# Performance work log

Measured on AMD Instinct MI355X. Metric: run time of the kernel, lower is better.

Reference implementation:

```python
import jax, jax.numpy as jnp
import numpy as np

T, M, K, B, H, L, V = 64, 256, 6, 256, 256, 128, 780
E = T * M
PAD = E  # padding slot in hidden buffer = Lorentz origin

def _to_lorentz_np(s):
    t = np.sqrt(1.0 + (s * s).sum(-1, keepdims=True))
    return np.concatenate([t, s], -1).astype(np.float32)

def setup_inputs() -> dict:
    rng = np.random.default_rng(0)
    def make_nei():
        idx = np.full((T, M, K), PAD, np.int64)
        w = np.zeros((T, M, K), np.float32)
        for t in range(T):
            deg = rng.integers(0, K + 1, size=M)
            if t == 0:
                deg[:] = 0  # no messages exist yet
            mask = np.arange(K)[None, :] < deg[:, None]
            cand = rng.integers(0, max(1, t * M), size=(M, K))  # only already-computed slots
            idx[t] = np.where(mask, cand, PAD)
            w[t] = mask.astype(np.float32)
            w[t, deg == 0, 0] = 1.0  # zero-neighbor case -> use origin padding (as in torch code)
        return idx.astype(np.int32), w
    nei_h_idx, nei_h_w = make_nei()
    nei_o_idx, nei_o_w = make_nei()
    return dict(
        wid=jnp.asarray(rng.integers(0, V, size=(T, M)), jnp.int32),
        nei_h_idx=jnp.asarray(nei_h_idx), nei_h_w=jnp.asarray(nei_h_w),
        nei_o_idx=jnp.asarray(nei_o_idx), nei_o_w=jnp.asarray(nei_o_w),
        batch_idx=jnp.asarray(rng.integers(0, B, size=(T, M)), jnp.int32),
        direction=jnp.asarray(rng.integers(0, 2, size=(T, M)), jnp.int32),
        pred_target=jnp.asarray(rng.integers(0, V, size=(T, M)), jnp.int32),
        root_wid=jnp.asarray(rng.integers(0, V, size=(B,)), jnp.int32),
        root_o_idx=jnp.asarray(rng.integers(0, E, size=(B, K)), jnp.int32),
        root_o_w=jnp.ones((B, K), jnp.float32),
        x_tree_vecs=jnp.asarray(_to_lorentz_np(rng.standard_normal((B, L - 1)) * 0.5)),
        embedding=jnp.asarray(_to_lorentz_np(rng.standard_normal((V, H - 1)) * 0.5)),
        W0=jnp.asarray(rng.standard_normal((H, H)) * 0.02, dtype=jnp.float32),
        b0=jnp.zeros((H,), jnp.float32),
        s0=jnp.asarray(np.log(10.0), jnp.float32),
        W1=jnp.asarray(rng.standard_normal((H, 2 * H - 1)) * 0.02, dtype=jnp.float32),
        b1=jnp.zeros((H,), jnp.float32),
        s1=jnp.asarray(np.log(10.0), jnp.float32),
        wcls=jnp.asarray(_to_lorentz_np(rng.standard_normal((V, H + L - 2)) * 0.5)),
        wbias=jnp.zeros((V,), jnp.float32),
        ucls=jnp.asarray(_to_lorentz_np(rng.standard_normal((2, 2 * H + L - 3)) * 0.5)),
        ubias=jnp.zeros((2,), jnp.float32),
    )

def _llinear(x, W, b, scale):
    # LorentzLinear: affine map, then rescale space part so output stays on the hyperboloid
    x = x @ W.T + b
    xs = x[..., 1:]
    time = jax.nn.sigmoid(x[..., :1]) * jnp.exp(scale) + 1.1
    sq = (time * time - 1.0) / jnp.clip((xs * xs).sum(-1, keepdims=True), 1e-8)
    return jnp.concatenate([time, xs * jnp.sqrt(sq)], -1)

def _mid_point(x, w):
    # Lorentz centroid: weighted mean renormalized to the manifold. x: [...,K,d], w: [...,K]
    ave = jnp.einsum('...k,...kd->...d', w, x) / jnp.clip(w.sum(-1, keepdims=True), 1e-8)
    inner = (ave[..., 1:] ** 2).sum(-1, keepdims=True) - ave[..., :1] ** 2  # <ave,ave>_L
    return ave / jnp.sqrt(jnp.clip(-inner, 1e-8))

def _concat(x, y):
    # hyperbolic concat: keep space parts, recompute time (dim = d1+d2-1)
    time = jnp.sqrt(jnp.clip(x[..., :1] ** 2 + y[..., :1] ** 2 - 1.0, 1e-8))
    return jnp.concatenate([time, x[..., 1:], y[..., 1:]], -1)

def _centroid(x, cls_pts, bias):
    # LorentzCentroidDistance logits: 2 + 2*<x, c>_L + bias
    inner = x[..., 1:] @ cls_pts[:, 1:].T - x[..., :1] * cls_pts[None, :, 0]
    return 2.0 + 2.0 * inner + bias

def _ce(scores, tgt):
    lp = jax.nn.log_softmax(scores, -1)
    return -jnp.take_along_axis(lp, tgt[:, None], axis=-1)[:, 0]

def _forward_core(wid, nei_h_idx, nei_h_w, nei_o_idx, nei_o_w, batch_idx, direction,
                  pred_target, root_wid, root_o_idx, root_o_w, x_tree_vecs, embedding,
                  W0, b0, s0, W1, b1, s1, wcls, wbias, ucls, ubias):
    hbuf0 = jnp.zeros((E + 1, H), jnp.float32).at[:, 0].set(1.0)  # all origin; slot E is padding

    def step(carry, xs_t):
        hbuf, t = carry
        wid_t, idx_t, w_t = xs_t
        cur_x = embedding[wid_t]                      # [M,H]
        h_nei = hbuf[idx_t]                           # [M,K,H] gather of prior messages
        h1 = _llinear(h_nei, W0, b0, s0)              # A0
        h1m = _mid_point(h1, w_t)                     # [M,H]
        new_h = _llinear(_concat(cur_x, h1m), W1, b1, s1)  # A1
        hbuf = jax.lax.dynamic_update_slice(hbuf, new_h, (t * M, 0))
        return (hbuf, t + jnp.int32(1)), new_h

    (hbuf, _), new_h = jax.lax.scan(step, (hbuf0, jnp.int32(0)), (wid, nei_h_idx, nei_h_w))
    new_h = new_h.reshape(E, H)
    cur_x = embedding[wid.reshape(E)]
    cur_o = _mid_point(hbuf[nei_o_idx.reshape(E, K)], nei_o_w.reshape(E, K))
    ctx = x_tree_vecs[batch_idx.reshape(E)]

    # word prediction: roots (origin hidden) + forward-direction messages
    origin = jnp.zeros((B, H), jnp.float32).at[:, 0].set(1.0)
    root_scores = _centroid(_concat(origin, x_tree_vecs), wcls, wbias)   # [B,V]
    msg_scores = _centroid(_concat(new_h, ctx), wcls, wbias)             # [E,V]
    pmask = direction.reshape(E).astype(jnp.float32)
    pt = pred_target.reshape(E)
    pred_loss = (_ce(root_scores, root_wid).sum() + (pmask * _ce(msg_scores, pt)).sum()) / B
    pred_hit = ((jnp.argmax(root_scores, -1) == root_wid).astype(jnp.float32).sum()
                + (pmask * (jnp.argmax(msg_scores, -1) == pt).astype(jnp.float32)).sum())
    pred_acc = pred_hit / (B + pmask.sum())

    # stop prediction: every message + final per-tree root entry (target 0)
    stop_h = _concat(_concat(cur_x, cur_o), ctx)                         # [E, 2H+L-2]
    root_o = _mid_point(hbuf[root_o_idx], root_o_w)
    stop_root = _concat(_concat(embedding[root_wid], root_o), x_tree_vecs)
    stop_scores = _centroid(jnp.concatenate([stop_h, stop_root], 0), ucls, ubias)
    stop_tgt = jnp.concatenate([direction.reshape(E), jnp.zeros((B,), jnp.int32)], 0)
    stop_loss = _ce(stop_scores, stop_tgt).sum() / B
    stop_acc = (jnp.argmax(stop_scores, -1) == stop_tgt).astype(jnp.float32).mean()
    return pred_loss, stop_loss, pred_acc, stop_acc

def reference(wid, nei_h_idx, nei_h_w, nei_o_idx, nei_o_w, batch_idx, direction,
              pred_target, root_wid, root_o_idx, root_o_w, x_tree_vecs, embedding,
              W0, b0, s0, W1, b1, s1, wcls, wbias, ucls, ubias):
    return _forward_core(wid, nei_h_idx, nei_h_w, nei_o_idx, nei_o_w, batch_idx, direction,
                         pred_target, root_wid, root_o_idx, root_o_w, x_tree_vecs, embedding,
                         W0, b0, s0, W1, b1, s1, wcls, wbias, ucls, ubias)
```

## Files before the change

### kernel.cpp

```cpp
#include <hip/hip_runtime.h>
#include <math.h>

#define T_ 64
#define M_ 256
#define K_ 6
#define B_ 256
#define H_ 256
#define L_ 128
#define V_ 780
#define E_ (T_*M_)
#define ZD 383
#define UD 638
#define KP 384
#define VP 832
#define TAG_PAD 0x7fffffffu

typedef unsigned short ushort_t;
typedef __attribute__((ext_vector_type(8))) _Float16 half8v;
typedef __attribute__((ext_vector_type(4))) _Float16 half4v;
typedef __attribute__((ext_vector_type(2))) _Float16 half2v;
typedef __attribute__((ext_vector_type(4))) float f32x4v;
typedef unsigned long long u64;


__device__ __forceinline__ float blk_sum(float v, float* red) {
    int j = threadIdx.x;
    #pragma unroll
    for (int o = 32; o > 0; o >>= 1) v += __shfl_down(v, o, 64);
    __syncthreads();
    if ((j & 63) == 0) red[j >> 6] = v;
    __syncthreads();
    return red[0] + red[1] + red[2] + red[3];
}

__device__ __forceinline__ float wave_sum(float v) {
    #pragma unroll
    for (int o = 32; o > 0; o >>= 1) v += __shfl_xor(v, o, 64);
    return v;
}

__device__ __forceinline__ _Float16 f2h(float x) { return (_Float16)x; }

__device__ __forceinline__ u64 llc_load8(const u64* p) {
    return __hip_atomic_load(p, __ATOMIC_RELAXED, __HIP_MEMORY_SCOPE_AGENT);
}
__device__ __forceinline__ void llc_store8(u64* p, u64 v) {
    __hip_atomic_store(p, v, __ATOMIC_RELAXED, __HIP_MEMORY_SCOPE_AGENT);
}


#define PREP_R0 H_
#define PREP_RT ((E_ + 1) * 128)
#define PREP_RH3 E_
#define PREP_R1 65536
#define PREP_R2 65536
#define PREP_R3 (VP * KP)
#define PREP_R4 65536
#define PREP_TOTAL (PREP_R0 + PREP_RT + PREP_RH3 + PREP_R1 + PREP_R2 + PREP_R3 + PREP_R4)

__global__ __launch_bounds__(256) void prep_k(const float* __restrict__ W0,
                                              const float* __restrict__ W1,
                                              const float* __restrict__ wcls,
                                              float* __restrict__ hbuf,
                                              u64* __restrict__ hbuf2,
                                              u64* __restrict__ hbuf3,
                                              _Float16* __restrict__ W0P,
                                              _Float16* __restrict__ W1HP,
                                              _Float16* __restrict__ Wh,
                                              float* __restrict__ W1T) {
    int idx = blockIdx.x * 256 + threadIdx.x;
    if (idx < PREP_R0) {
        hbuf[(size_t)E_ * H_ + idx] = (idx == 0) ? 1.f : 0.f;
        return;
    }
    idx -= PREP_R0;
    if (idx < PREP_RT) {
        int row = idx >> 7, cp = idx & 127;
        u64 val = 0ull;
        if (row == E_) {
            unsigned int lo = (cp == 0) ? 0x3C00u : 0u;
            val = ((u64)TAG_PAD << 32) | lo;
        }
        hbuf2[idx] = val;
        return;
    }
    idx -= PREP_RT;
    if (idx < PREP_RH3) {
        hbuf3[idx] = 0ull;
        return;
    }
    idx -= PREP_RH3;
    if (idx < PREP_R1) {
        int e = idx & 7, l = (idx >> 3) & 63, ks = (idx >> 9) & 7, nt = idx >> 12;
        int jj = nt * 16 + (l & 15);
        int ii = ks * 32 + (l >> 4) * 8 + e;
        W0P[idx] = f2h(W0[(size_t)jj * H_ + ii]);
        return;
    }
    idx -= PREP_R1;
    if (idx < PREP_R2) {
        int e = idx & 7, l = (idx >> 3) & 63, ks = (idx >> 9) & 7, nt = idx >> 12;
        int jj = nt * 16 + (l & 15);
        int ii = ks * 32 + (l >> 4) * 8 + e;
        float v = (ii == 0) ? W1[(size_t)jj * (2 * H_ - 1)]
                            : W1[(size_t)jj * (2 * H_ - 1) + 255 + ii];
        W1HP[idx] = f2h(v);
        return;
    }
    idx -= PREP_R2;
    if (idx < PREP_R3) {
        int v = idx / KP, k = idx - v * KP;
        float val = (v < V_ && k < ZD) ? wcls[(size_t)v * ZD + k] : 0.f;
        Wh[idx] = f2h(val);
        return;
    }
    idx -= PREP_R3;
    if (idx < PREP_R4) {
        int i = idx >> 8, j = idx & 255;
        W1T[idx] = (i >= 1) ? W1[(size_t)j * (2 * H_ - 1) + i] : 0.f;
    }
}


__global__ __launch_bounds__(256) void basew_k(const float* __restrict__ emb,
                                               const float* __restrict__ W1T,
                                               const float* __restrict__ b1,
                                               float* __restrict__ basew) {
    int v = blockIdx.x, j = threadIdx.x;
    __shared__ float cxs[256];
    cxs[j] = emb[(size_t)v * H_ + j];
    __syncthreads();
    float acc = b1[j];
    #pragma unroll 8
    for (int i = 1; i < 256; i++) acc = fmaf(cxs[i], W1T[i * 256 + j], acc);
    basew[(size_t)v * H_ + j] = acc;
}


__global__ __launch_bounds__(256, 1) void scan_flow(float* __restrict__ hbuf,
        u64* __restrict__ hbuf2, u64* __restrict__ hbuf3,
        const _Float16* __restrict__ W0P, const float* __restrict__ b0, const float* __restrict__ s0p,
        const _Float16* __restrict__ W1HP, const float* __restrict__ s1p,
        const float* __restrict__ emb, const int* __restrict__ wid,
        const int* __restrict__ nhi, const float* __restrict__ nhw,
        const float* __restrict__ basew,
        const _Float16* __restrict__ Wh, const float* __restrict__ wbias,
        const int* __restrict__ pt, const int* __restrict__ dir,
        const int* __restrict__ bidx, const float* __restrict__ xtv,
        float* __restrict__ part) {
    int tid = threadIdx.x;
    int w = tid >> 6, l = tid & 63;
    int quad = l >> 4, col = l & 15;
    int m = blockIdx.x;
    int j0 = 4 * l;
    int cp = tid & 127;
    int rsel = tid >> 7;

    __shared__ __align__(16) _Float16 hn16[16][264];
    __shared__ __align__(16) _Float16 zzs[4][264];
    __shared__ __align__(16) float Ys[6][256];
    __shared__ __align__(16) float y2s[256];
    __shared__ __align__(16) _Float16 As[64][392];
    __shared__ __align__(16) _Float16 Bsf[64][392];
    __shared__ __align__(16) float SCs[64][68];
    __shared__ float rmax[64], rsum[64], rval[64];
    __shared__ int   rargi[64];

    half8v w0f[4][8], w1f[4][8];
    #pragma unroll
    for (int q = 0; q < 4; q++) {
        int nt = 4 * w + q;
        #pragma unroll
        for (int ks = 0; ks < 8; ks++) {
            w0f[q][ks] = *(const half8v*)(W0P + ((size_t)(nt * 8 + ks) * 64 + l) * 8);
            w1f[q][ks] = *(const half8v*)(W1HP + ((size_t)(nt * 8 + ks) * 64 + l) * 8);
        }
    }

    float es0 = expf(s0p[0]);
    float es1 = expf(s1p[0]);
    float4 bj4 = *(const float4*)(b0 + j0);

    unsigned int tagx[3];
    const u64* pp[3];
    u64 pvv[3];
    #pragma unroll
    for (int p = 0; p < 3; p++) {
        int row = 2 * p + rsel;
        int id = nhi[(size_t)m * K_ + row];
        tagx[p] = (id < E_) ? (unsigned int)(id >> 8) + 1u : TAG_PAD;
        pp[p] = hbuf2 + ((size_t)id << 7) + cp;
        pvv[p] = llc_load8(pp[p]);
    }

    for (int t = 0; t < T_; t++) {
        int e = t * M_ + m;
        const float* wp = nhw + e * K_;

        float wk[K_];
        #pragma unroll
        for (int k = 0; k < K_; k++) wk[k] = wp[k];
        int wde = wid[e];
        float4 bw4 = *(const float4*)(basew + (size_t)wde * H_ + j0);
        float cx0 = emb[(size_t)wde * H_];

        for (;;) {
            bool ok = ((unsigned int)(pvv[0] >> 32) == tagx[0])
                   && ((unsigned int)(pvv[1] >> 32) == tagx[1])
                   && ((unsigned int)(pvv[2] >> 32) == tagx[2]);
            if (ok) break;
            __builtin_amdgcn_s_sleep(1);
            #pragma unroll
            for (int p = 0; p < 3; p++)
                if ((unsigned int)(pvv[p] >> 32) != tagx[p]) pvv[p] = llc_load8(pp[p]);
        }
        #pragma unroll
        for (int p = 0; p < 3; p++)
            *(unsigned int*)&hn16[2 * p + rsel][cp * 2] = (unsigned int)pvv[p];
        __syncthreads();

        if (t + 1 < T_) {
            #pragma unroll
            for (int p = 0; p < 3; p++) {
                int row = 2 * p + rsel;
                int id = nhi[(size_t)(e + M_) * K_ + row];
                tagx[p] = (id < E_) ? (unsigned int)(id >> 8) + 1u : TAG_PAD;
                pp[p] = hbuf2 + ((size_t)id << 7) + cp;
                pvv[p] = llc_load8(pp[p]);
            }
        }

        f32x4v acc[4];
        #pragma unroll
        for (int q = 0; q < 4; q++) acc[q] = (f32x4v){0.f, 0.f, 0.f, 0.f};
        #pragma unroll
        for (int ks = 0; ks < 8; ks++) {
            half8v afr = *(const half8v*)&hn16[col][ks * 32 + quad * 8];
            #pragma unroll
            for (int q = 0; q < 4; q++)
                acc[q] = __builtin_amdgcn_mfma_f32_16x16x32_f16(afr, w0f[q][ks], acc[q], 0, 0, 0);
        }
        #pragma unroll
        for (int q = 0; q < 4; q++) {
            int nt = 4 * w + q;
            #pragma unroll
            for (int rr = 0; rr < 4; rr++) {
                int row = quad * 4 + rr;
                if (row < 6) Ys[row][nt * 16 + col] = acc[q][rr];
            }
        }
        __syncthreads();

        float y[K_][4];
        #pragma unroll
        for (int k = 0; k < K_; k++) {
            float4 yv = *(const float4*)&Ys[k][j0];
            y[k][0] = yv.x + bj4.x; y[k][1] = yv.y + bj4.y;
            y[k][2] = yv.z + bj4.z; y[k][3] = yv.w + bj4.w;
        }
        float c[K_];
        #pragma unroll
        for (int k = 0; k < K_; k++) {
            float cc = y[k][0] * y[k][0] + y[k][1] * y[k][1]
                     + y[k][2] * y[k][2] + y[k][3] * y[k][3];
            if (l == 0) cc -= y[k][0] * y[k][0];
            c[k] = cc;
        }
        #pragma unroll
        for (int o = 32; o > 0; o >>= 1) {
            #pragma unroll
            for (int k = 0; k < K_; k++) c[k] += __shfl_xor(c[k], o, 64);
        }
        float y0b[K_];
        #pragma unroll
        for (int k = 0; k < K_; k++) y0b[k] = __shfl(y[k][0], 0, 64);

        float ave[4] = {0.f, 0.f, 0.f, 0.f};
        float wsum = 0.f;
        #pragma unroll
        for (int k = 0; k < K_; k++) {
            float tm = es0 / (1.f + expf(-y0b[k])) + 1.1f;
            float sc = sqrtf((tm * tm - 1.f) / fmaxf(c[k], 1e-8f));
            #pragma unroll
            for (int c2 = 0; c2 < 4; c2++) {
                float h1v = (l == 0 && c2 == 0) ? tm : y[k][c2] * sc;
                ave[c2] += wk[k] * h1v;
            }
            wsum += wk[k];
        }
        float inv = 1.f / fmaxf(wsum, 1e-8f);
        float innl = 0.f;
        #pragma unroll
        for (int c2 = 0; c2 < 4; c2++) { ave[c2] *= inv; innl += ave[c2] * ave[c2]; }
        if (l == 0) innl -= 2.f * ave[0] * ave[0];
        float inner = wave_sum(innl);
        float rsc = 1.f / sqrtf(fmaxf(-inner, 1e-8f));

        #pragma unroll
        for (int c2 = 0; c2 < 4; c2++) {
            int j = j0 + c2;
            float h1m = ave[c2] * rsc;
            if (j == 0) {
                zzs[w][0] = f2h(sqrtf(fmaxf(cx0 * cx0 + h1m * h1m - 1.f, 1e-8f)));
            } else {
                zzs[w][j] = f2h(h1m);
            }
        }

        f32x4v a2[4];
        #pragma unroll
        for (int q = 0; q < 4; q++) a2[q] = (f32x4v){0.f, 0.f, 0.f, 0.f};
        #pragma unroll
        for (int ks = 0; ks < 8; ks++) {
            half8v zfr = *(const half8v*)&zzs[w][ks * 32 + quad * 8];
            #pragma unroll
            for (int q = 0; q < 4; q++)
                a2[q] = __builtin_amdgcn_mfma_f32_16x16x32_f16(zfr, w1f[q][ks], a2[q], 0, 0, 0);
        }
        if (quad == 0) {
            #pragma unroll
            for (int q = 0; q < 4; q++) y2s[(4 * w + q) * 16 + col] = a2[q][0];
        }
        __syncthreads();

        if (w == 0) {
            float4 y2v = *(const float4*)&y2s[j0];
            float y2[4] = {y2v.x + bw4.x, y2v.y + bw4.y, y2v.z + bw4.z, y2v.w + bw4.w};
            float c2s = y2[0] * y2[0] + y2[1] * y2[1] + y2[2] * y2[2] + y2[3] * y2[3];
            if (l == 0) c2s -= y2[0] * y2[0];
            float ssq2 = wave_sum(c2s);
            float y20 = __shfl(y2[0], 0, 64);
            float tm2 = es1 / (1.f + expf(-y20)) + 1.1f;
            float sc2 = sqrtf((tm2 * tm2 - 1.f) / fmaxf(ssq2, 1e-8f));
            float hv0 = (l == 0) ? tm2 : y2[0] * sc2;
            float hv1 = y2[1] * sc2, hv2 = y2[2] * sc2, hv3 = y2[3] * sc2;

            unsigned int tag = (unsigned int)t + 1u;
            union { half2v h; unsigned int u; } c01, c23;
            c01.h.x = f2h(hv0); c01.h.y = f2h(hv1);
            c23.h.x = f2h(hv2); c23.h.y = f2h(hv3);
            u64* pb = hbuf2 + ((size_t)e << 7) + 2 * l;
            llc_store8(pb,     ((u64)tag << 32) | c01.u);
            llc_store8(pb + 1, ((u64)tag << 32) | c23.u);

            if (l == 0) {
                union { float f; unsigned int u; } h0b; h0b.f = tm2;
                llc_store8(hbuf3 + e, ((u64)tag << 32) | h0b.u);
            }

            float4 out4 = {hv0, hv1, hv2, hv3};
            *(float4*)(hbuf + (size_t)e * H_ + j0) = out4;
        }
    }

    {
        int m0 = m * 64;

        u64 gpv[32];
        #pragma unroll
        for (int i = 0; i < 32; i++) {
            int p = tid + i * 256;
            int row = p >> 7, cpp = p & 127;
            gpv[i] = llc_load8(hbuf2 + ((size_t)(m0 + row) << 7) + cpp);
        }
        for (;;) {
            bool ok = true;
            #pragma unroll
            for (int i = 0; i < 32; i++) {
                int row = (tid + i * 256) >> 7;
                unsigned int tg = (unsigned int)((m0 + row) >> 8) + 1u;
                if ((unsigned int)(gpv[i] >> 32) != tg) ok = false;
            }
            if (ok) break;
            __builtin_amdgcn_s_sleep(1);
            #pragma unroll
            for (int i = 0; i < 32; i++) {
                int p = tid + i * 256;
                int row = p >> 7, cpp = p & 127;
                unsigned int tg = (unsigned int)((m0 + row) >> 8) + 1u;
                if ((unsigned int)(gpv[i] >> 32) != tg)
                    gpv[i] = llc_load8(hbuf2 + ((size_t)(m0 + row) << 7) + cpp);
            }
        }
        #pragma unroll
        for (int i = 0; i < 32; i++) {
            int p = tid + i * 256;
            int row = p >> 7, cpp = p & 127;
            *(unsigned int*)&As[row][2 * cpp] = (unsigned int)gpv[i];
        }
        #pragma unroll
        for (int i = 0; i < 16; i++) {
            int p = tid + i * 256;
            int row = p >> 6, k2 = (p & 63) * 2;
            int bi = bidx[m0 + row];
            int ca = 256 + k2;
            half2v hv;
            hv.x = (ca <= 382) ? f2h(xtv[(size_t)bi * L_ + (ca - 255)]) : (_Float16)0.f;
            hv.y = (ca + 1 <= 382) ? f2h(xtv[(size_t)bi * L_ + (ca - 254)]) : (_Float16)0.f;
            *(half2v*)&As[row][ca] = hv;
        }
        if (tid < 64) {
            int e2 = m0 + tid;
            unsigned int tg = (unsigned int)(e2 >> 8) + 1u;
            u64 hv3 = llc_load8(hbuf3 + e2);
            while ((unsigned int)(hv3 >> 32) != tg) {
                __builtin_amdgcn_s_sleep(1);
                hv3 = llc_load8(hbuf3 + e2);
            }
            union { unsigned int u; float f; } h0c; h0c.u = (unsigned int)hv3;
            int bi = bidx[e2];
            float c0 = xtv[(size_t)bi * L_];
            float z0 = sqrtf(fmaxf(h0c.f * h0c.f + c0 * c0 - 1.f, 1e-8f));
            As[tid][0] = f2h(-z0);
            rmax[tid] = -1e30f; rsum[tid] = 0.f; rargi[tid] = 0; rval[tid] = 0.f;
        }
        __syncthreads();

        int q8 = quad * 8;
        for (int nt = 0; nt < 13; nt++) {
            int n0 = nt * 64;
            #pragma unroll
            for (int i = 0; i < 12; i++) {
                int uu = tid + i * 256;
                int row = uu / 48, c8 = (uu % 48) * 8;
                *(uint4*)&Bsf[row][c8] = *(const uint4*)(Wh + (size_t)(n0 + row) * KP + c8);
            }
            __syncthreads();

            f32x4v gacc[4];
            #pragma unroll
            for (int mt = 0; mt < 4; mt++) gacc[mt] = (f32x4v){0.f, 0.f, 0.f, 0.f};
            #pragma unroll
            for (int ks = 0; ks < 12; ks++) {
                half8v bfr = *(const half8v*)&Bsf[w * 16 + col][ks * 32 + q8];
                #pragma unroll
                for (int mt = 0; mt < 4; mt++) {
                    half8v afr = *(const half8v*)&As[mt * 16 + col][ks * 32 + q8];
                    gacc[mt] = __builtin_amdgcn_mfma_f32_16x16x32_f16(afr, bfr, gacc[mt], 0, 0, 0);
                }
            }
            int ncol = n0 + w * 16 + col;
            float bias = (ncol < V_) ? wbias[ncol] : 0.f;
            #pragma unroll
            for (int mt = 0; mt < 4; mt++) {
                #pragma unroll
                for (int rr = 0; rr < 4; rr++)
                    SCs[mt * 16 + quad * 4 + rr][w * 16 + col] = 2.f + 2.f * gacc[mt][rr] + bias;
            }
            __syncthreads();

            {
                int row = tid >> 2, prt = tid & 3;
                int tg = pt[m0 + row];
                float vals[16];
                float lm = -1e30f; int li = 0;
                #pragma unroll
                for (int cc = 0; cc < 16; cc++) {
                    int nc = n0 + prt * 16 + cc;
                    float x = (nc < V_) ? SCs[row][prt * 16 + cc] : -1e30f;
                    vals[cc] = x;
                    if (x > lm) { lm = x; li = nc; }
                    if (nc == tg) rval[row] = x;
                }
                #pragma unroll
                for (int o = 1; o < 4; o <<= 1) {
                    float om = __shfl_xor(lm, o, 64);
                    int   oi = __shfl_xor(li, o, 64);
                    if (om > lm || (om == lm && oi < li)) { lm = om; li = oi; }
                }
                float ls = 0.f;
                #pragma unroll
                for (int cc = 0; cc < 16; cc++) {
                    int nc = n0 + prt * 16 + cc;
                    if (nc < V_) ls += expf(vals[cc] - lm);
                }
                #pragma unroll
                for (int o = 1; o < 4; o <<= 1) ls += __shfl_xor(ls, o, 64);
                if (prt == 0) {
                    float om = rmax[row], os = rsum[row];
                    float nm = fmaxf(om, lm);
                    rsum[row] = os * expf(om - nm) + ls * expf(lm - nm);
                    if (lm > om) rargi[row] = li;
                    rmax[row] = nm;
                }
            }
            __syncthreads();
        }

        if (tid < 64) {
            int e2 = m0 + tid;
            int tg = pt[e2];
            float pm = (float)dir[e2];
            float lse = rmax[tid] + logf(rsum[tid]);
            float lloss = pm * (lse - rval[tid]);
            float lhit  = pm * ((rargi[tid] == tg) ? 1.f : 0.f);
            float lpm   = pm;
            lloss = wave_sum(lloss);
            lhit  = wave_sum(lhit);
            lpm   = wave_sum(lpm);
            if (tid == 0) {
                float* pr = part + (size_t)m * 8;
                pr[0] = lloss; pr[1] = lhit; pr[2] = lpm;
                pr[3] = 0.f; pr[4] = 0.f;
            }
        }
    }
}


__global__ __launch_bounds__(256) void stoproot_k(const float* __restrict__ hbuf,
        const float* __restrict__ emb, const float* __restrict__ xtv,
        const int* __restrict__ wid, const int* __restrict__ noi, const float* __restrict__ now_w,
        const int* __restrict__ bidx, const int* __restrict__ dir,
        const int* __restrict__ rwid, const int* __restrict__ roi, const float* __restrict__ row_w,
        const float* __restrict__ wcls, const float* __restrict__ wbias,
        const float* __restrict__ ucls, const float* __restrict__ ubias,
        float* __restrict__ part) {
    __shared__ float red[256];
    __shared__ int   redi[256];
    __shared__ float shs[4];
    __shared__ float ctxs[L_];
    __shared__ float sc[V_];
    __shared__ float red2[4][2];

    if (blockIdx.x < 256) {
        int w = threadIdx.x >> 6, l = threadIdx.x & 63;
        int wg = blockIdx.x * 4 + w;

        float ua0[4], ub0[4], ua1[4], ub1[4], uc0[2], uc1[2];
        #pragma unroll
        for (int s = 0; s < 4; s++) {
            int j = s * 64 + l;
            ua0[s] = ucls[j];        ub0[s] = ucls[255 + j];
            ua1[s] = ucls[UD + j];   ub1[s] = ucls[UD + 255 + j];
        }
        #pragma unroll
        for (int s = 0; s < 2; s++) {
            int j = s * 64 + l;
            uc0[s] = ucls[510 + j];  uc1[s] = ucls[UD + 510 + j];
        }
        float u00 = ucls[0], u10 = ucls[UD];
        float ubs0 = ubias[0], ubs1 = ubias[1];

        float lloss = 0.f, lhit = 0.f;
        for (int i = 0; i < 16; i++) {
            int e = wg * 16 + i;
            const int*   ip = noi + e * K_;
            const float* wp = now_w + e * K_;
            float ave[4] = {0.f, 0.f, 0.f, 0.f};
            float wsum = 0.f;
            #pragma unroll
            for (int k = 0; k < K_; k++) {
                int id = ip[k]; float wt = wp[k];
                wsum += wt;
                const float* hr = hbuf + (size_t)id * H_;
                #pragma unroll
                for (int s = 0; s < 4; s++) ave[s] += wt * hr[s * 64 + l];
            }
            float inv = 1.f / fmaxf(wsum, 1e-8f);
            float innl = 0.f;
            #pragma unroll
            for (int s = 0; s < 4; s++) { ave[s] *= inv; innl += ave[s] * ave[s]; }
            if (l == 0) innl -= 2.f * ave[0] * ave[0];
            float inner = wave_sum(innl);
            float cs = 1.f / sqrtf(fmaxf(-inner, 1e-8f));

            int we = wid[e], bi = bidx[e];
            const float* er = emb + (size_t)we * H_;
            const float* cr = xtv + (size_t)bi * L_;

            float p0 = 0.f, p1 = 0.f;
            #pragma unroll
            for (int s = 0; s < 4; s++) {
                float cx = er[s * 64 + l];
                float co = ave[s] * cs;
                if (s == 0 && l == 0) {
                    float ctx0 = cr[0];
                    float t1sq = fmaxf(cx * cx + co * co - 1.f, 1e-8f);
                    float sh0 = sqrtf(fmaxf(t1sq + ctx0 * ctx0 - 1.f, 1e-8f));
                    p0 += -sh0 * u00; p1 += -sh0 * u10;
                } else {
                    p0 += cx * ua0[s] + co * ub0[s];
                    p1 += cx * ua1[s] + co * ub1[s];
                }
                if (s < 2) {
                    int j = s * 64 + l;
                    if (j >= 1) {
                        float ctx = cr[j];
                        p0 += ctx * uc0[s]; p1 += ctx * uc1[s];
                    }
                }
            }
            p0 = wave_sum(p0); p1 = wave_sum(p1);
            if (l == 0) {
                float sc0 = 2.f + 2.f * p0 + ubs0;
                float sc1 = 2.f + 2.f * p1 + ubs1;
                int tgt = dir[e];
                float mm = fmaxf(sc0, sc1);
                float lse = mm + logf(expf(sc0 - mm) + expf(sc1 - mm));
                lloss += lse - ((tgt == 0) ? sc0 : sc1);
                int am = (sc1 > sc0) ? 1 : 0;
                lhit += (am == tgt) ? 1.f : 0.f;
            }
        }
        if (l == 0) { red2[w][0] = lloss; red2[w][1] = lhit; }
        __syncthreads();
        if (threadIdx.x == 0) {
            float* pr = part + (size_t)(256 + blockIdx.x) * 8;
            pr[0] = 0.f; pr[1] = 0.f; pr[2] = 0.f;
            pr[3] = red2[0][0] + red2[1][0] + red2[2][0] + red2[3][0];
            pr[4] = red2[0][1] + red2[1][1] + red2[2][1] + red2[3][1];
        }
    } else {
        int b = blockIdx.x - 256, j = threadIdx.x;
        float* pr = part + (size_t)(512 + b) * 8;

        const int*   ip = roi + b * K_;
        const float* wp = row_w + b * K_;
        float ave = 0.f, wsum = 0.f;
        #pragma unroll
        for (int k = 0; k < K_; k++) {
            int id = ip[k]; float w = wp[k];
            ave += w * hbuf[(size_t)id * H_ + j];
            wsum += w;
        }
        ave /= fmaxf(wsum, 1e-8f);
        float inner = blk_sum((j == 0) ? -ave * ave : ave * ave, red);
        float ro = ave / sqrtf(fmaxf(-inner, 1e-8f));

        int   rw = rwid[b];
        float er = emb[(size_t)rw * H_ + j];
        float ctxj = (j < L_) ? xtv[(size_t)b * L_ + j] : 0.f;
        if (j == 0) { shs[0] = er; shs[1] = ro; shs[2] = ctxj; }
        if (j < L_) ctxs[j] = ctxj;
        __syncthreads();
        float t1sq = fmaxf(shs[0] * shs[0] + shs[1] * shs[1] - 1.f, 1e-8f);
        float sh0  = sqrtf(fmaxf(t1sq + shs[2] * shs[2] - 1.f, 1e-8f));

        float p0, p1;
        if (j >= 1) {
            p0 = er * ucls[j] + ro * ucls[255 + j];
            p1 = er * ucls[UD + j] + ro * ucls[UD + 255 + j];
            if (j < L_) { p0 += ctxj * ucls[510 + j]; p1 += ctxj * ucls[UD + 510 + j]; }
        } else {
            p0 = -sh0 * ucls[0];
            p1 = -sh0 * ucls[UD];
        }
        float s0 = 2.f + 2.f * blk_sum(p0, red) + ubias[0];
        float s1 = 2.f + 2.f * blk_sum(p1, red) + ubias[1];
        if (j == 0) {
            float mm = fmaxf(s0, s1);
            float lse = mm + logf(expf(s0 - mm) + expf(s1 - mm));
            int am = (s1 > s0) ? 1 : 0;
            pr[3] = lse - s0;
            pr[4] = (am == 0) ? 1.f : 0.f;
        }

        float c0 = shs[2];
        float z0 = sqrtf(fmaxf(c0 * c0, 1e-8f));
        __syncthreads();
        for (int v = j; v < V_; v += 256) {
            const float* wv = wcls + (size_t)v * ZD;
            float d = -z0 * wv[0];
            for (int i = 1; i < L_; i++) d += ctxs[i] * wv[255 + i];
            sc[v] = 2.f + 2.f * d + wbias[v];
        }
        __syncthreads();
        float mx = -1e30f; int mi = 0;
        for (int v = j; v < V_; v += 256) { float x = sc[v]; if (x > mx) { mx = x; mi = v; } }
        red[j] = mx; redi[j] = mi;
        __syncthreads();
        for (int o = 128; o > 0; o >>= 1) {
            if (j < o) {
                float xo = red[j + o]; int io = redi[j + o];
                if (xo > red[j] || (xo == red[j] && io < redi[j])) { red[j] = xo; redi[j] = io; }
            }
            __syncthreads();
        }
        float gm = red[0]; int ga = redi[0];
        __syncthreads();
        float se = 0.f;
        for (int v = j; v < V_; v += 256) se += expf(sc[v] - gm);
        red[j] = se;
        __syncthreads();
        for (int o = 128; o > 0; o >>= 1) { if (j < o) red[j] += red[j + o]; __syncthreads(); }
        if (j == 0) {
            float lse = gm + logf(red[0]);
            pr[0] = lse - sc[rw];
            pr[1] = (ga == rw) ? 1.f : 0.f;
            pr[2] = 0.f;
        }
    }
}


__global__ __launch_bounds__(256) void finalize2(const float* __restrict__ part,
                                                 float* __restrict__ out) {
    int j = threadIdx.x;
    __shared__ float red[256][5];
    #pragma unroll
    for (int c = 0; c < 5; c++)
        red[j][c] = part[(size_t)j * 8 + c] + part[(size_t)(j + 256) * 8 + c]
                  + part[(size_t)(j + 512) * 8 + c];
    __syncthreads();
    for (int o = 128; o > 0; o >>= 1) {
        if (j < o) {
            #pragma unroll
            for (int c = 0; c < 5; c++) red[j][c] += red[j + o][c];
        }
        __syncthreads();
    }
    if (j == 0) {
        out[0] = red[0][0] / (float)B_;
        out[1] = red[0][3] / (float)B_;
        out[2] = red[0][1] / ((float)B_ + red[0][2]);
        out[3] = red[0][4] / (float)(E_ + B_);
    }
}


extern "C" void kernel_launch(void* const* d_in, const int* in_sizes, int n_in,
                              void* d_out, int out_size, void* d_ws, size_t ws_size,
                              hipStream_t stream) {
    const int*   wid   = (const int*)d_in[0];
    const int*   nhi   = (const int*)d_in[1];
    const float* nhw   = (const float*)d_in[2];
    const int*   noi   = (const int*)d_in[3];
    const float* now_w = (const float*)d_in[4];
    const int*   bidx  = (const int*)d_in[5];
    const int*   dir   = (const int*)d_in[6];
    const int*   pt    = (const int*)d_in[7];
    const int*   rwid  = (const int*)d_in[8];
    const int*   roi   = (const int*)d_in[9];
    const float* row_w = (const float*)d_in[10];
    const float* xtv   = (const float*)d_in[11];
    const float* emb   = (const float*)d_in[12];
    const float* W0    = (const float*)d_in[13];
    const float* b0    = (const float*)d_in[14];
    const float* s0    = (const float*)d_in[15];
    const float* W1    = (const float*)d_in[16];
    const float* b1    = (const float*)d_in[17];
    const float* s1    = (const float*)d_in[18];
    const float* wcls  = (const float*)d_in[19];
    const float* wbias = (const float*)d_in[20];
    const float* ucls  = (const float*)d_in[21];
    const float* ubias = (const float*)d_in[22];

    float* ws    = (float*)d_ws;
    float* hbuf  = ws;
    u64*   hbuf2 = (u64*)(hbuf + (size_t)(E_ + 1) * H_);
    u64*   hbuf3 = hbuf2 + (size_t)(E_ + 1) * 128;
    float* part  = (float*)(hbuf3 + E_);
    float* basew = part + 768 * 8;
    float* W1T   = basew + (size_t)V_ * H_;
    _Float16* W0P  = (_Float16*)(W1T + 65536);
    _Float16* W1HP = W0P + 65536;
    _Float16* Wh   = W1HP + 65536;
    float* out  = (float*)d_out;

    prep_k<<<(PREP_TOTAL + 255) / 256, 256, 0, stream>>>(W0, W1, wcls, hbuf, hbuf2, hbuf3,
                                                         W0P, W1HP, Wh, W1T);
    basew_k<<<V_, 256, 0, stream>>>(emb, W1T, b1, basew);

    scan_flow<<<M_, 256, 0, stream>>>(hbuf, hbuf2, hbuf3, W0P, b0, s0, W1HP, s1,
                                      emb, wid, nhi, nhw, basew,
                                      Wh, wbias, pt, dir, bidx, xtv, part);

    stoproot_k<<<512, 256, 0, stream>>>(hbuf, emb, xtv, wid, noi, now_w, bidx, dir,
                                        rwid, roi, row_w, wcls, wbias, ucls, ubias, part);
    finalize2<<<1, 256, 0, stream>>>(part, out);
}
```

Baseline: 575.4 us.

## Unify hidden state into tagged fp32 buffer and fuse stop/root into scan kernel

Replaces the three hidden-state buffers (fp32 hbuf, fp16-packed tagged hbuf2, tagged h0 hbuf3) with a single tagged buffer holding one fp32 value per 64-bit word. The stop/root kernel is merged into the scan kernel, using tag polling instead of a kernel boundary, and the basew computation is folded into prep_k, which reads W1 directly without a transpose. This removes two launches, duplicate stores, and the fp16 packing. In exchange the tagged buffer doubles in size, so each neighbor gather reads twice as many bytes, and the fused stop phase adds polling inside the serial scan kernel.

```diff
diff --git a/kernel.cpp b/kernel.cpp
--- a/kernel.cpp
+++ b/kernel.cpp
@@ -15,9 +15,7 @@
 #define VP 832
 #define TAG_PAD 0x7fffffffu
 
-typedef unsigned short ushort_t;
 typedef __attribute__((ext_vector_type(8))) _Float16 half8v;
-typedef __attribute__((ext_vector_type(4))) _Float16 half4v;
 typedef __attribute__((ext_vector_type(2))) _Float16 half2v;
 typedef __attribute__((ext_vector_type(4))) float f32x4v;
 typedef unsigned long long u64;
@@ -49,56 +47,53 @@
 }
 
 
-#define PREP_R0 H_
-#define PREP_RT ((E_ + 1) * 128)
-#define PREP_RH3 E_
-#define PREP_R1 65536
-#define PREP_R2 65536
-#define PREP_R3 (VP * KP)
-#define PREP_R4 65536
-#define PREP_TOTAL (PREP_R0 + PREP_RT + PREP_RH3 + PREP_R1 + PREP_R2 + PREP_R3 + PREP_R4)
+#define S_BW (V_ * H_)
+#define S_T4 ((E_ + 1) * 256)
+#define S_W0 65536
+#define S_W1 65536
+#define S_WH (VP * KP)
+#define S_TOTAL (S_BW + S_T4 + S_W0 + S_W1 + S_WH)
 
 __global__ __launch_bounds__(256) void prep_k(const float* __restrict__ W0,
-                                              const float* __restrict__ W1,
-                                              const float* __restrict__ wcls,
-                                              float* __restrict__ hbuf,
-                                              u64* __restrict__ hbuf2,
-                                              u64* __restrict__ hbuf3,
-                                              _Float16* __restrict__ W0P,
-                                              _Float16* __restrict__ W1HP,
-                                              _Float16* __restrict__ Wh,
-                                              float* __restrict__ W1T) {
+        const float* __restrict__ W1, const float* __restrict__ wcls,
+        const float* __restrict__ emb, const float* __restrict__ b1,
+        u64* __restrict__ hbuf4, _Float16* __restrict__ W0P,
+        _Float16* __restrict__ W1HP, _Float16* __restrict__ Wh,
+        float* __restrict__ basew) {
+    __shared__ float cxs[256];
     int idx = blockIdx.x * 256 + threadIdx.x;
-    if (idx < PREP_R0) {
-        hbuf[(size_t)E_ * H_ + idx] = (idx == 0) ? 1.f : 0.f;
+    if (idx < S_BW) {
+        int v = idx >> 8, j = idx & 255;
+        cxs[threadIdx.x] = emb[(size_t)v * H_ + threadIdx.x];
+        __syncthreads();
+        float acc = b1[j];
+        const float* w1r = W1 + (size_t)j * (2 * H_ - 1);
+        #pragma unroll 8
+        for (int i = 1; i < 256; i++) acc = fmaf(cxs[i], w1r[i], acc);
+        basew[idx] = acc;
         return;
     }
-    idx -= PREP_R0;
-    if (idx < PREP_RT) {
-        int row = idx >> 7, cp = idx & 127;
+    idx -= S_BW;
+    if (idx < S_T4) {
+        int row = idx >> 8, c = idx & 255;
         u64 val = 0ull;
         if (row == E_) {
-            unsigned int lo = (cp == 0) ? 0x3C00u : 0u;
+            unsigned int lo = (c == 0) ? 0x3f800000u : 0u;
             val = ((u64)TAG_PAD << 32) | lo;
         }
-        hbuf2[idx] = val;
+        hbuf4[idx] = val;
         return;
     }
-    idx -= PREP_RT;
-    if (idx < PREP_RH3) {
-        hbuf3[idx] = 0ull;
-        return;
-    }
-    idx -= PREP_RH3;
-    if (idx < PREP_R1) {
+    idx -= S_T4;
+    if (idx < S_W0) {
         int e = idx & 7, l = (idx >> 3) & 63, ks = (idx >> 9) & 7, nt = idx >> 12;
         int jj = nt * 16 + (l & 15);
         int ii = ks * 32 + (l >> 4) * 8 + e;
         W0P[idx] = f2h(W0[(size_t)jj * H_ + ii]);
         return;
     }
-    idx -= PREP_R1;
-    if (idx < PREP_R2) {
+    idx -= S_W0;
+    if (idx < S_W1) {
         int e = idx & 7, l = (idx >> 3) & 63, ks = (idx >> 9) & 7, nt = idx >> 12;
         int jj = nt * 16 + (l & 15);
         int ii = ks * 32 + (l >> 4) * 8 + e;
@@ -107,38 +102,16 @@
         W1HP[idx] = f2h(v);
         return;
     }
-    idx -= PREP_R2;
-    if (idx < PREP_R3) {
+    idx -= S_W1;
+    if (idx < S_WH) {
         int v = idx / KP, k = idx - v * KP;
         float val = (v < V_ && k < ZD) ? wcls[(size_t)v * ZD + k] : 0.f;
         Wh[idx] = f2h(val);
-        return;
-    }
-    idx -= PREP_R3;
-    if (idx < PREP_R4) {
-        int i = idx >> 8, j = idx & 255;
-        W1T[idx] = (i >= 1) ? W1[(size_t)j * (2 * H_ - 1) + i] : 0.f;
     }
 }
 
 
-__global__ __launch_bounds__(256) void basew_k(const float* __restrict__ emb,
-                                               const float* __restrict__ W1T,
-                                               const float* __restrict__ b1,
-                                               float* __restrict__ basew) {
-    int v = blockIdx.x, j = threadIdx.x;
-    __shared__ float cxs[256];
-    cxs[j] = emb[(size_t)v * H_ + j];
-    __syncthreads();
-    float acc = b1[j];
-    #pragma unroll 8
-    for (int i = 1; i < 256; i++) acc = fmaf(cxs[i], W1T[i * 256 + j], acc);
-    basew[(size_t)v * H_ + j] = acc;
-}
-
-
-__global__ __launch_bounds__(256, 1) void scan_flow(float* __restrict__ hbuf,
-        u64* __restrict__ hbuf2, u64* __restrict__ hbuf3,
+__global__ __launch_bounds__(256, 1) void scan_flow(u64* __restrict__ hbuf4,
         const _Float16* __restrict__ W0P, const float* __restrict__ b0, const float* __restrict__ s0p,
         const _Float16* __restrict__ W1HP, const float* __restrict__ s1p,
         const float* __restrict__ emb, const int* __restrict__ wid,
@@ -147,14 +120,17 @@
         const _Float16* __restrict__ Wh, const float* __restrict__ wbias,
         const int* __restrict__ pt, const int* __restrict__ dir,
         const int* __restrict__ bidx, const float* __restrict__ xtv,
+        const int* __restrict__ noi, const float* __restrict__ now_w,
+        const int* __restrict__ rwid, const int* __restrict__ roi,
+        const float* __restrict__ row_w,
+        const float* __restrict__ wcls, const float* __restrict__ ucls,
+        const float* __restrict__ ubias,
         float* __restrict__ part) {
     int tid = threadIdx.x;
     int w = tid >> 6, l = tid & 63;
     int quad = l >> 4, col = l & 15;
     int m = blockIdx.x;
     int j0 = 4 * l;
-    int cp = tid & 127;
-    int rsel = tid >> 7;
 
     __shared__ __align__(16) _Float16 hn16[16][264];
     __shared__ __align__(16) _Float16 zzs[4][264];
@@ -165,6 +141,12 @@
     __shared__ __align__(16) float SCs[64][68];
     __shared__ float rmax[64], rsum[64], rval[64];
     __shared__ int   rargi[64];
+    __shared__ float red[256];
+    __shared__ int   redi[256];
+    __shared__ float shs[4];
+    __shared__ float ctxs[L_];
+    __shared__ float sc[V_];
+    __shared__ float red2[4][2];
 
     half8v w0f[4][8], w1f[4][8];
     #pragma unroll
@@ -181,16 +163,13 @@
     float es1 = expf(s1p[0]);
     float4 bj4 = *(const float4*)(b0 + j0);
 
-    unsigned int tagx[3];
-    const u64* pp[3];
-    u64 pvv[3];
+    unsigned tagr[K_]; const u64* rp[K_]; u64 pv6[K_];
     #pragma unroll
-    for (int p = 0; p < 3; p++) {
-        int row = 2 * p + rsel;
-        int id = nhi[(size_t)m * K_ + row];
-        tagx[p] = (id < E_) ? (unsigned int)(id >> 8) + 1u : TAG_PAD;
-        pp[p] = hbuf2 + ((size_t)id << 7) + cp;
-        pvv[p] = llc_load8(pp[p]);
+    for (int r = 0; r < K_; r++) {
+        int id = nhi[(size_t)m * K_ + r];
+        tagr[r] = (id < E_) ? (unsigned)(id >> 8) + 1u : TAG_PAD;
+        rp[r] = hbuf4 + ((size_t)id << 8) + tid;
+        pv6[r] = llc_load8(rp[r]);
     }
 
     for (int t = 0; t < T_; t++) {
@@ -205,28 +184,30 @@
         float cx0 = emb[(size_t)wde * H_];
 
         for (;;) {
-            bool ok = ((unsigned int)(pvv[0] >> 32) == tagx[0])
-                   && ((unsigned int)(pvv[1] >> 32) == tagx[1])
-                   && ((unsigned int)(pvv[2] >> 32) == tagx[2]);
+            bool ok = true;
+            #pragma unroll
+            for (int r = 0; r < K_; r++)
+                if ((unsigned)(pv6[r] >> 32) != tagr[r]) ok = false;
             if (ok) break;
             __builtin_amdgcn_s_sleep(1);
             #pragma unroll
-            for (int p = 0; p < 3; p++)
-                if ((unsigned int)(pvv[p] >> 32) != tagx[p]) pvv[p] = llc_load8(pp[p]);
-        }
-        #pragma unroll
-        for (int p = 0; p < 3; p++)
-            *(unsigned int*)&hn16[2 * p + rsel][cp * 2] = (unsigned int)pvv[p];
+            for (int r = 0; r < K_; r++)
+                if ((unsigned)(pv6[r] >> 32) != tagr[r]) pv6[r] = llc_load8(rp[r]);
+        }
+        #pragma unroll
+        for (int r = 0; r < K_; r++) {
+            union { unsigned u; float f; } cv; cv.u = (unsigned)pv6[r];
+            hn16[r][tid] = f2h(cv.f);
+        }
         __syncthreads();
 
         if (t + 1 < T_) {
             #pragma unroll
-            for (int p = 0; p < 3; p++) {
-                int row = 2 * p + rsel;
-                int id = nhi[(size_t)(e + M_) * K_ + row];
-                tagx[p] = (id < E_) ? (unsigned int)(id >> 8) + 1u : TAG_PAD;
-                pp[p] = hbuf2 + ((size_t)id << 7) + cp;
-                pvv[p] = llc_load8(pp[p]);
+            for (int r = 0; r < K_; r++) {
+                int id = nhi[(size_t)(e + M_) * K_ + r];
+                tagr[r] = (id < E_) ? (unsigned)(id >> 8) + 1u : TAG_PAD;
+                rp[r] = hbuf4 + ((size_t)id << 8) + tid;
+                pv6[r] = llc_load8(rp[r]);
             }
         }
 
@@ -280,10 +261,10 @@
         #pragma unroll
         for (int k = 0; k < K_; k++) {
             float tm = es0 / (1.f + expf(-y0b[k])) + 1.1f;
-            float sc = sqrtf((tm * tm - 1.f) / fmaxf(c[k], 1e-8f));
+            float scv = sqrtf((tm * tm - 1.f) / fmaxf(c[k], 1e-8f));
             #pragma unroll
             for (int c2 = 0; c2 < 4; c2++) {
-                float h1v = (l == 0 && c2 == 0) ? tm : y[k][c2] * sc;
+                float h1v = (l == 0 && c2 == 0) ? tm : y[k][c2] * scv;
                 ave[c2] += wk[k] * h1v;
             }
             wsum += wk[k];
@@ -335,58 +316,50 @@
             float hv0 = (l == 0) ? tm2 : y2[0] * sc2;
             float hv1 = y2[1] * sc2, hv2 = y2[2] * sc2, hv3 = y2[3] * sc2;
 
-            unsigned int tag = (unsigned int)t + 1u;
-            union { half2v h; unsigned int u; } c01, c23;
-            c01.h.x = f2h(hv0); c01.h.y = f2h(hv1);
-            c23.h.x = f2h(hv2); c23.h.y = f2h(hv3);
-            u64* pb = hbuf2 + ((size_t)e << 7) + 2 * l;
-            llc_store8(pb,     ((u64)tag << 32) | c01.u);
-            llc_store8(pb + 1, ((u64)tag << 32) | c23.u);
-
-            if (l == 0) {
-                union { float f; unsigned int u; } h0b; h0b.f = tm2;
-                llc_store8(hbuf3 + e, ((u64)tag << 32) | h0b.u);
-            }
-
-            float4 out4 = {hv0, hv1, hv2, hv3};
-            *(float4*)(hbuf + (size_t)e * H_ + j0) = out4;
-        }
-    }
-
+            u64 tb = (u64)((unsigned)t + 1u) << 32;
+            union { float f; unsigned u; } q0, q1, q2, q3;
+            q0.f = hv0; q1.f = hv1; q2.f = hv2; q3.f = hv3;
+            u64* p4 = hbuf4 + ((size_t)e << 8) + j0;
+            llc_store8(p4,     tb | q0.u);
+            llc_store8(p4 + 1, tb | q1.u);
+            llc_store8(p4 + 2, tb | q2.u);
+            llc_store8(p4 + 3, tb | q3.u);
+        }
+    }
+
+    int m0 = m * 64;
     {
-        int m0 = m * 64;
-
-        u64 gpv[32];
-        #pragma unroll
-        for (int i = 0; i < 32; i++) {
-            int p = tid + i * 256;
-            int row = p >> 7, cpp = p & 127;
-            gpv[i] = llc_load8(hbuf2 + ((size_t)(m0 + row) << 7) + cpp);
-        }
-        for (;;) {
-            bool ok = true;
-            #pragma unroll
-            for (int i = 0; i < 32; i++) {
-                int row = (tid + i * 256) >> 7;
-                unsigned int tg = (unsigned int)((m0 + row) >> 8) + 1u;
-                if ((unsigned int)(gpv[i] >> 32) != tg) ok = false;
-            }
-            if (ok) break;
-            __builtin_amdgcn_s_sleep(1);
-            #pragma unroll
-            for (int i = 0; i < 32; i++) {
-                int p = tid + i * 256;
-                int row = p >> 7, cpp = p & 127;
-                unsigned int tg = (unsigned int)((m0 + row) >> 8) + 1u;
-                if ((unsigned int)(gpv[i] >> 32) != tg)
-                    gpv[i] = llc_load8(hbuf2 + ((size_t)(m0 + row) << 7) + cpp);
-            }
-        }
-        #pragma unroll
-        for (int i = 0; i < 32; i++) {
-            int p = tid + i * 256;
-            int row = p >> 7, cpp = p & 127;
-            *(unsigned int*)&As[row][2 * cpp] = (unsigned int)gpv[i];
+        for (int bb = 0; bb < 4; bb++) {
+            u64 gp[16];
+            #pragma unroll
+            for (int i = 0; i < 16; i++) {
+                int row = bb * 16 + i;
+                gp[i] = llc_load8(hbuf4 + ((size_t)(m0 + row) << 8) + tid);
+            }
+            for (;;) {
+                bool ok = true;
+                #pragma unroll
+                for (int i = 0; i < 16; i++) {
+                    int row = bb * 16 + i;
+                    unsigned tg = (unsigned)((m0 + row) >> 8) + 1u;
+                    if ((unsigned)(gp[i] >> 32) != tg) ok = false;
+                }
+                if (ok) break;
+                __builtin_amdgcn_s_sleep(1);
+                #pragma unroll
+                for (int i = 0; i < 16; i++) {
+                    int row = bb * 16 + i;
+                    unsigned tg = (unsigned)((m0 + row) >> 8) + 1u;
+                    if ((unsigned)(gp[i] >> 32) != tg)
+                        gp[i] = llc_load8(hbuf4 + ((size_t)(m0 + row) << 8) + tid);
+                }
+            }
+            #pragma unroll
+            for (int i = 0; i < 16; i++) {
+                int row = bb * 16 + i;
+                union { unsigned u; float f; } cv; cv.u = (unsigned)gp[i];
+                As[row][tid] = f2h(cv.f);
+            }
         }
         #pragma unroll
         for (int i = 0; i < 16; i++) {
@@ -399,15 +372,16 @@
             hv.y = (ca + 1 <= 382) ? f2h(xtv[(size_t)bi * L_ + (ca - 254)]) : (_Float16)0.f;
             *(half2v*)&As[row][ca] = hv;
         }
+        __syncthreads();
         if (tid < 64) {
             int e2 = m0 + tid;
-            unsigned int tg = (unsigned int)(e2 >> 8) + 1u;
-            u64 hv3 = llc_load8(hbuf3 + e2);
-            while ((unsigned int)(hv3 >> 32) != tg) {
+            unsigned tg = (unsigned)(e2 >> 8) + 1u;
+            u64 hv3 = llc_load8(hbuf4 + ((size_t)e2 << 8));
+            while ((unsigned)(hv3 >> 32) != tg) {
                 __builtin_amdgcn_s_sleep(1);
-                hv3 = llc_load8(hbuf3 + e2);
-            }
-            union { unsigned int u; float f; } h0c; h0c.u = (unsigned int)hv3;
+                hv3 = llc_load8(hbuf4 + ((size_t)e2 << 8));
+            }
+            union { unsigned u; float f; } h0c; h0c.u = (unsigned)hv3;
             int bi = bidx[e2];
             float c0 = xtv[(size_t)bi * L_];
             float z0 = sqrtf(fmaxf(h0c.f * h0c.f + c0 * c0 - 1.f, 1e-8f));
@@ -505,28 +479,10 @@
             }
         }
     }
-}
-
-
-__global__ __launch_bounds__(256) void stoproot_k(const float* __restrict__ hbuf,
-        const float* __restrict__ emb, const float* __restrict__ xtv,
-        const int* __restrict__ wid, const int* __restrict__ noi, const float* __restrict__ now_w,
-        const int* __restrict__ bidx, const int* __restrict__ dir,
-        const int* __restrict__ rwid, const int* __restrict__ roi, const float* __restrict__ row_w,
-        const float* __restrict__ wcls, const float* __restrict__ wbias,
-        const float* __restrict__ ucls, const float* __restrict__ ubias,
-        float* __restrict__ part) {
-    __shared__ float red[256];
-    __shared__ int   redi[256];
-    __shared__ float shs[4];
-    __shared__ float ctxs[L_];
-    __shared__ float sc[V_];
-    __shared__ float red2[4][2];
-
-    if (blockIdx.x < 256) {
-        int w = threadIdx.x >> 6, l = threadIdx.x & 63;
-        int wg = blockIdx.x * 4 + w;
-
+    __syncthreads();
+
+    {
+        int wg = m * 4 + w;
         float ua0[4], ub0[4], ua1[4], ub1[4], uc0[2], uc1[2];
         #pragma unroll
         for (int s = 0; s < 4; s++) {
@@ -544,18 +500,48 @@
 
         float lloss = 0.f, lhit = 0.f;
         for (int i = 0; i < 16; i++) {
-            int e = wg * 16 + i;
-            const int*   ip = noi + e * K_;
-            const float* wp = now_w + e * K_;
+            int e2 = wg * 16 + i;
+            const int*   ip  = noi + e2 * K_;
+            const float* wpp = now_w + e2 * K_;
+
+            const u64* bp[K_];
+            unsigned tgk[K_];
+            u64 hv[K_][4];
+            #pragma unroll
+            for (int k = 0; k < K_; k++) {
+                int id = ip[k];
+                tgk[k] = (id < E_) ? (unsigned)(id >> 8) + 1u : TAG_PAD;
+                bp[k] = hbuf4 + ((size_t)id << 8) + l;
+                #pragma unroll
+                for (int s = 0; s < 4; s++) hv[k][s] = llc_load8(bp[k] + s * 64);
+            }
+            for (;;) {
+                bool ok = true;
+                #pragma unroll
+                for (int k = 0; k < K_; k++)
+                    #pragma unroll
+                    for (int s = 0; s < 4; s++)
+                        if ((unsigned)(hv[k][s] >> 32) != tgk[k]) ok = false;
+                if (ok) break;
+                __builtin_amdgcn_s_sleep(1);
+                #pragma unroll
+                for (int k = 0; k < K_; k++)
+                    #pragma unroll
+                    for (int s = 0; s < 4; s++)
+                        if ((unsigned)(hv[k][s] >> 32) != tgk[k])
+                            hv[k][s] = llc_load8(bp[k] + s * 64);
+            }
+
             float ave[4] = {0.f, 0.f, 0.f, 0.f};
             float wsum = 0.f;
             #pragma unroll
             for (int k = 0; k < K_; k++) {
-                int id = ip[k]; float wt = wp[k];
-                wsum += wt;
-                const float* hr = hbuf + (size_t)id * H_;
-                #pragma unroll
-                for (int s = 0; s < 4; s++) ave[s] += wt * hr[s * 64 + l];
+                float wt = wpp[k]; wsum += wt;
+                #pragma unroll
+                for (int s = 0; s < 4; s++) {
+                    union { unsigned u; float f; } cv; cv.u = (unsigned)hv[k][s];
+                    ave[s] += wt * cv.f;
+                }
             }
             float inv = 1.f / fmaxf(wsum, 1e-8f);
             float innl = 0.f;
@@ -565,7 +551,7 @@
             float inner = wave_sum(innl);
             float cs = 1.f / sqrtf(fmaxf(-inner, 1e-8f));
 
-            int we = wid[e], bi = bidx[e];
+            int we = wid[e2], bi = bidx[e2];
             const float* er = emb + (size_t)we * H_;
             const float* cr = xtv + (size_t)bi * L_;
 
@@ -595,7 +581,7 @@
             if (l == 0) {
                 float sc0 = 2.f + 2.f * p0 + ubs0;
                 float sc1 = 2.f + 2.f * p1 + ubs1;
-                int tgt = dir[e];
+                int tgt = dir[e2];
                 float mm = fmaxf(sc0, sc1);
                 float lse = mm + logf(expf(sc0 - mm) + expf(sc1 - mm));
                 lloss += lse - ((tgt == 0) ? sc0 : sc1);
@@ -605,24 +591,46 @@
         }
         if (l == 0) { red2[w][0] = lloss; red2[w][1] = lhit; }
         __syncthreads();
-        if (threadIdx.x == 0) {
-            float* pr = part + (size_t)(256 + blockIdx.x) * 8;
+        if (tid == 0) {
+            float* pr = part + (size_t)(256 + m) * 8;
             pr[0] = 0.f; pr[1] = 0.f; pr[2] = 0.f;
             pr[3] = red2[0][0] + red2[1][0] + red2[2][0] + red2[3][0];
             pr[4] = red2[0][1] + red2[1][1] + red2[2][1] + red2[3][1];
         }
-    } else {
-        int b = blockIdx.x - 256, j = threadIdx.x;
+    }
+    __syncthreads();
+
+    {
+        int b = m, j = tid;
         float* pr = part + (size_t)(512 + b) * 8;
 
-        const int*   ip = roi + b * K_;
-        const float* wp = row_w + b * K_;
+        const int*   ip  = roi + b * K_;
+        const float* wpp = row_w + b * K_;
+        const u64* bp[K_]; unsigned tgk[K_]; u64 hv[K_];
+        #pragma unroll
+        for (int k = 0; k < K_; k++) {
+            int id = ip[k];
+            tgk[k] = (unsigned)(id >> 8) + 1u;
+            bp[k] = hbuf4 + ((size_t)id << 8) + j;
+            hv[k] = llc_load8(bp[k]);
+        }
+        for (;;) {
+            bool ok = true;
+            #pragma unroll
+            for (int k = 0; k < K_; k++)
+                if ((unsigned)(hv[k] >> 32) != tgk[k]) ok = false;
+            if (ok) break;
+            __builtin_amdgcn_s_sleep(1);
+            #pragma unroll
+            for (int k = 0; k < K_; k++)
+                if ((unsigned)(hv[k] >> 32) != tgk[k]) hv[k] = llc_load8(bp[k]);
+        }
         float ave = 0.f, wsum = 0.f;
         #pragma unroll
         for (int k = 0; k < K_; k++) {
-            int id = ip[k]; float w = wp[k];
-            ave += w * hbuf[(size_t)id * H_ + j];
-            wsum += w;
+            union { unsigned u; float f; } cv; cv.u = (unsigned)hv[k];
+            float wt = wpp[k];
+            ave += wt * cv.f; wsum += wt;
         }
         ave /= fmaxf(wsum, 1e-8f);
         float inner = blk_sum((j == 0) ? -ave * ave : ave * ave, red);
@@ -746,27 +754,22 @@
     const float* ucls  = (const float*)d_in[21];
     const float* ubias = (const float*)d_in[22];
 
-    float* ws    = (float*)d_ws;
-    float* hbuf  = ws;
-    u64*   hbuf2 = (u64*)(hbuf + (size_t)(E_ + 1) * H_);
-    u64*   hbuf3 = hbuf2 + (size_t)(E_ + 1) * 128;
-    float* part  = (float*)(hbuf3 + E_);
+    u64*   hbuf4 = (u64*)d_ws;
+    float* part  = (float*)(hbuf4 + (size_t)(E_ + 1) * 256);
     float* basew = part + 768 * 8;
-    float* W1T   = basew + (size_t)V_ * H_;
-    _Float16* W0P  = (_Float16*)(W1T + 65536);
+    _Float16* W0P  = (_Float16*)(basew + (size_t)V_ * H_);
     _Float16* W1HP = W0P + 65536;
     _Float16* Wh   = W1HP + 65536;
     float* out  = (float*)d_out;
 
-    prep_k<<<(PREP_TOTAL + 255) / 256, 256, 0, stream>>>(W0, W1, wcls, hbuf, hbuf2, hbuf3,
-                                                         W0P, W1HP, Wh, W1T);
-    basew_k<<<V_, 256, 0, stream>>>(emb, W1T, b1, basew);
-
-    scan_flow<<<M_, 256, 0, stream>>>(hbuf, hbuf2, hbuf3, W0P, b0, s0, W1HP, s1,
+    prep_k<<<S_TOTAL / 256, 256, 0, stream>>>(W0, W1, wcls, emb, b1,
+                                              hbuf4, W0P, W1HP, Wh, basew);
+
+    scan_flow<<<M_, 256, 0, stream>>>(hbuf4, W0P, b0, s0, W1HP, s1,
                                       emb, wid, nhi, nhw, basew,
-                                      Wh, wbias, pt, dir, bidx, xtv, part);
-
-    stoproot_k<<<512, 256, 0, stream>>>(hbuf, emb, xtv, wid, noi, now_w, bidx, dir,
-                                        rwid, roi, row_w, wcls, wbias, ucls, ubias, part);
+                                      Wh, wbias, pt, dir, bidx, xtv,
+                                      noi, now_w, rwid, roi, row_w,
+                                      wcls, ucls, ubias, part);
+
     finalize2<<<1, 256, 0, stream>>>(part, out);
 }
```

Result: slower. 607.3 us (+5.5%).
